# Kernel tuning notes

Measured on AMD Instinct MI355X. Metric: run time of the kernel, lower is better.

## Reference

```python
import jax, jax.numpy as jnp
import numpy as np

PIECES = 64  # self.plane


def _proj(f, w1, b1, w2, b2):
    # Projection: fc2(relu(fc1(f))), final_relu=False
    h = jax.nn.relu(f @ w1 + b1)
    return h @ w2 + b2


def _cf(img, param, pieces):
    # img: [B,3,H,W], param: [B,3,P]
    # total[b,c,h,w] = sum_i clamp(img - i/P, 0, 1/P) * param[b,c,i], then * P / sum_i param
    grid = jnp.arange(pieces, dtype=img.dtype) / pieces            # [P]
    clipped = jnp.clip(img[..., None] - grid, 0.0, 1.0 / pieces)   # [B,3,H,W,P]
    total = jnp.einsum('bchwp,bcp->bchw', clipped, param)
    norm = pieces / (jnp.sum(param, axis=-1) + 1e-30)              # [B,3]
    return total * norm[:, :, None, None]


def setup_inputs() -> dict:
    key = jax.random.key(0)
    ks = jax.random.split(key, 11)
    B, H, W = 8, 256, 256
    s = 0.05
    return {
        'x': jax.random.uniform(ks[0], (B, 3, H, W), jnp.float32),
        'f_feature': jax.random.normal(ks[1], (B, 512), jnp.float32),
        'b_feature': jax.random.normal(ks[2], (B, 512), jnp.float32),
        # stacked weights for [fc_f_1, fc_b_1, fc_f_s, fc_b_s]
        'proj_w1': jax.random.normal(ks[3], (4, 512, 192), jnp.float32) * s,
        'proj_b1': jax.random.normal(ks[4], (4, 192), jnp.float32) * s,
        'proj_w2': jax.random.normal(ks[5], (4, 192, 192), jnp.float32) * s,
        'proj_b2': jax.random.normal(ks[6], (4, 192), jnp.float32) * s,
        'fc_w1': jax.random.normal(ks[7], (576, 192), jnp.float32) * s,
        'fc_b1': jax.random.normal(ks[8], (192,), jnp.float32) * s,
        'fc_w2': jax.random.normal(ks[9], (192, 192), jnp.float32) * s,
        'fc_b2': jax.random.normal(ks[10], (192,), jnp.float32) * s,
    }


def reference(x, f_feature, b_feature, proj_w1, proj_b1, proj_w2, proj_b2,
              fc_w1, fc_b1, fc_w2, fc_b2):
    B = x.shape[0]
    # rgb_to_grayscale with 3 output channels (ITU-R 601 weights)
    gw = jnp.array([0.299, 0.587, 0.114], dtype=x.dtype)
    gray = jnp.broadcast_to(jnp.einsum('bchw,c->bhw', x, gw)[:, None], x.shape)

    # four stacked Projections: inputs [f, b, f, b]
    feats = jnp.stack([f_feature, b_feature, f_feature, b_feature])       # [4,B,512]
    h = jax.nn.relu(jnp.einsum('kbi,kio->kbo', feats, proj_w1) + proj_b1[:, None, :])
    outs = jnp.einsum('kbo,koq->kbq', h, proj_w2) + proj_b2[:, None, :]   # [4,B,192]
    param_f, param_b = outs[0], outs[1]
    param_s = outs[2] + outs[3]

    cat = jnp.concatenate([param_f, param_b, param_s], axis=1)            # [B,576]
    param = _proj(cat, fc_w1, fc_b1, fc_w2, fc_b2)                        # [B,192]

    p_all = param.reshape(B, 3, PIECES)
    p_f = param_f.reshape(B, 3, PIECES)
    p_b = param_b.reshape(B, 3, PIECES)

    return (_cf(x, p_all, PIECES), _cf(gray, p_f, PIECES), _cf(gray, p_b, PIECES))
```

## Files before the change

### kernel.cpp

```cpp
#include <hip/hip_runtime.h>

#define HWSZ 65536
#define PLANE (3 * HWSZ)
#define OUTSTRIDE (8 * PLANE)
#define MAGIC 0x13572468

__global__ __launch_bounds__(384) void k_mlp(
    const float* __restrict__ f, const float* __restrict__ bf,
    const float* __restrict__ pw1, const float* __restrict__ pb1,
    const float* __restrict__ pw2, const float* __restrict__ pb2,
    const float* __restrict__ fw1, const float* __restrict__ fb1,
    const float* __restrict__ fw2, const float* __restrict__ fb2,
    float* __restrict__ ws) {
  __shared__ float smem[2304];
  int t = threadIdx.x, blk = blockIdx.x;

  float* outs  = ws;
  float* hc    = ws + 12288;
  float* param = ws + 13824;
  int* fbase = (int*)(ws + 16384);

  int k = blk >> 3, b = blk & 7;
  {
    int q = t % 48, s = t / 48;
    float* sf  = smem;
    float* red = smem + 512;
    float* sh  = smem + 2048;

    const float* feat = ((k & 1) ? bf : f) + b * 512;
    for (int i = t; i < 512; i += 384) sf[i] = feat[i];
    __syncthreads();

    {
      const float4* w = (const float4*)(pw1 + (size_t)k * (512 * 192));
      float4 acc = {0.f, 0.f, 0.f, 0.f};
      int i0 = s * 64;
      for (int r = 0; r < 4; ++r) {
        float4 wv[16];
#pragma unroll
        for (int j = 0; j < 16; ++j)
          wv[j] = w[(size_t)(i0 + r * 16 + j) * 48 + q];
#pragma unroll
        for (int j = 0; j < 16; ++j) {
          float v = sf[i0 + r * 16 + j];
          acc.x = fmaf(v, wv[j].x, acc.x); acc.y = fmaf(v, wv[j].y, acc.y);
          acc.z = fmaf(v, wv[j].z, acc.z); acc.w = fmaf(v, wv[j].w, acc.w);
        }
      }
      ((float4*)(red + s * 192))[q] = acc;
    }
    __syncthreads();
    if (t < 192) {
      float a = pb1[k * 192 + t];
#pragma unroll
      for (int s2 = 0; s2 < 8; ++s2) a += red[s2 * 192 + t];
      sh[t] = fmaxf(a, 0.f);
    }
    __syncthreads();
    {
      const float4* w = (const float4*)(pw2 + (size_t)k * (192 * 192));
      float4 acc = {0.f, 0.f, 0.f, 0.f};
      int i0 = s * 24;
      for (int r = 0; r < 2; ++r) {
        float4 wv[12];
#pragma unroll
        for (int j = 0; j < 12; ++j)
          wv[j] = w[(size_t)(i0 + r * 12 + j) * 48 + q];
#pragma unroll
        for (int j = 0; j < 12; ++j) {
          float v = sh[i0 + r * 12 + j];
          acc.x = fmaf(v, wv[j].x, acc.x); acc.y = fmaf(v, wv[j].y, acc.y);
          acc.z = fmaf(v, wv[j].z, acc.z); acc.w = fmaf(v, wv[j].w, acc.w);
        }
      }
      ((float4*)(red + s * 192))[q] = acc;
    }
    __syncthreads();
    if (t < 192) {
      float a = pb2[k * 192 + t];
#pragma unroll
      for (int s2 = 0; s2 < 8; ++s2) a += red[s2 * 192 + t];
      outs[(k * 8 + b) * 192 + t] = a;
    }
    __syncthreads();
    if (t == 0) {
      __threadfence();
      atomicExch(&fbase[blk * 16], MAGIC);
    }
  }

  int b2 = blk & 7, c4 = blk >> 3, ob2 = c4 * 48;
  int q = t % 12, s = t / 12;

  float4 wv1[18];
  {
    const float4* w = (const float4*)fw1;
    int i0 = s * 18;
#pragma unroll
    for (int j = 0; j < 18; ++j)
      wv1[j] = w[(size_t)(i0 + j) * 48 + (ob2 >> 2) + q];
  }

  if (t < 4) {
    while (atomicAdd(&fbase[(t * 8 + b2) * 16], 0) != MAGIC)
      __builtin_amdgcn_s_sleep(2);
  }
  __syncthreads();
  if (t == 0) __threadfence();
  __syncthreads();

  {
    float* sc  = smem;
    float* red = smem + 576;
    for (int idx = t; idx < 576; idx += 384) {
      float v;
      if (idx < 192)      v = outs[(0 * 8 + b2) * 192 + idx];
      else if (idx < 384) v = outs[(1 * 8 + b2) * 192 + (idx - 192)];
      else                v = outs[(2 * 8 + b2) * 192 + (idx - 384)] +
                              outs[(3 * 8 + b2) * 192 + (idx - 384)];
      sc[idx] = v;
    }
    __syncthreads();
    float4 acc = {0.f, 0.f, 0.f, 0.f};
    int i0 = s * 18;
#pragma unroll
    for (int j = 0; j < 18; ++j) {
      float v = sc[i0 + j];
      acc.x = fmaf(v, wv1[j].x, acc.x); acc.y = fmaf(v, wv1[j].y, acc.y);
      acc.z = fmaf(v, wv1[j].z, acc.z); acc.w = fmaf(v, wv1[j].w, acc.w);
    }
    ((float4*)(red + s * 48))[q] = acc;
    __syncthreads();
    if (t < 48) {
      float a = fb1[ob2 + t];
#pragma unroll
      for (int s2 = 0; s2 < 32; ++s2) a += red[s2 * 48 + t];
      hc[b2 * 192 + ob2 + t] = fmaxf(a, 0.f);
    }
    __syncthreads();
    if (t == 0) {
      __threadfence();
      atomicExch(&fbase[(64 + blk) * 16], MAGIC);
    }
  }

  float4 wv2[6];
  {
    const float4* w = (const float4*)fw2;
    int i0 = s * 6;
#pragma unroll
    for (int j = 0; j < 6; ++j)
      wv2[j] = w[(size_t)(i0 + j) * 48 + (ob2 >> 2) + q];
  }

  if (t < 4) {
    while (atomicAdd(&fbase[(64 + t * 8 + b2) * 16], 0) != MAGIC)
      __builtin_amdgcn_s_sleep(2);
  }
  __syncthreads();
  if (t == 0) __threadfence();
  __syncthreads();

  {
    float* sh  = smem;
    float* red = smem + 576;
    if (t < 192) sh[t] = hc[b2 * 192 + t];
    __syncthreads();
    float4 acc = {0.f, 0.f, 0.f, 0.f};
    int i0 = s * 6;
#pragma unroll
    for (int j = 0; j < 6; ++j) {
      float v = sh[i0 + j];
      acc.x = fmaf(v, wv2[j].x, acc.x); acc.y = fmaf(v, wv2[j].y, acc.y);
      acc.z = fmaf(v, wv2[j].z, acc.z); acc.w = fmaf(v, wv2[j].w, acc.w);
    }
    ((float4*)(red + s * 48))[q] = acc;
    __syncthreads();
    if (t < 48) {
      float a = fb2[ob2 + t];
#pragma unroll
      for (int s2 = 0; s2 < 32; ++s2) a += red[s2 * 48 + t];
      param[b2 * 192 + ob2 + t] = a;
    }
  }
}

__global__ __launch_bounds__(256) void k_render(
    const float* __restrict__ x, const float* __restrict__ ws,
    float* __restrict__ out) {
  int b = blockIdx.y, t = threadIdx.x;
  int wave = t >> 6, lane = t & 63;
  const float* outs  = ws;
  const float* param = ws + 13824;
  __shared__ float2 tab[576];

  int s4a = blockIdx.x * 512 + t, s4b = s4a + 256;
  const float* xb = x + (size_t)b * PLANE;
  float4 vr0 = ((const float4*)(xb))[s4a];
  float4 vr1 = ((const float4*)(xb))[s4b];
  float4 vg0 = ((const float4*)(xb + HWSZ))[s4a];
  float4 vg1 = ((const float4*)(xb + HWSZ))[s4b];
  float4 vb0 = ((const float4*)(xb + 2 * HWSZ))[s4a];
  float4 vb1 = ((const float4*)(xb + 2 * HWSZ))[s4b];

  for (int cur = wave; cur < 9; cur += 4) {
    int oi = cur / 3, c = cur - oi * 3;
    const float* src = (oi == 0) ? param + b * 192 + c * 64
                                 : outs + ((oi - 1) * 8 + b) * 192 + c * 64;
    float p = src[lane];
    float v = p;
#pragma unroll
    for (int d = 1; d < 64; d <<= 1) {
      float n = __shfl_up(v, d, 64);
      if (lane >= d) v += n;
    }
    float total = __shfl(v, 63, 64);
    float norm = 64.f / (total + 1e-30f);
    tab[cur * 64 + lane] = make_float2((v - p) * 0.015625f * norm, p * norm);
  }
  __syncthreads();

  auto idx_of = [&](float v, int& kk, float& tt) {
    int k = (int)(v * 64.f);
    k = k < 0 ? 0 : (k > 63 ? 63 : k);
    kk = k;
    tt = v - (float)k * 0.015625f;
  };
  auto evk = [&](int cur, int k, float tt) -> float {
    float2 e = tab[cur * 64 + k];
    return fmaf(tt, e.y, e.x);
  };
  auto ev4 = [&](int cur, float4 v) -> float4 {
    int k; float tt; float4 r;
    idx_of(v.x, k, tt); r.x = evk(cur, k, tt);
    idx_of(v.y, k, tt); r.y = evk(cur, k, tt);
    idx_of(v.z, k, tt); r.z = evk(cur, k, tt);
    idx_of(v.w, k, tt); r.w = evk(cur, k, tt);
    return r;
  };

  float* o0 = out + (size_t)b * PLANE;
  float* o1 = out + OUTSTRIDE + (size_t)b * PLANE;
  float* o2 = out + 2 * OUTSTRIDE + (size_t)b * PLANE;

  auto process = [&](int s4, float4 vr, float4 vg, float4 vb) {
    float4 gr;
    gr.x = fmaf(0.299f, vr.x, fmaf(0.587f, vg.x, 0.114f * vb.x));
    gr.y = fmaf(0.299f, vr.y, fmaf(0.587f, vg.y, 0.114f * vb.y));
    gr.z = fmaf(0.299f, vr.z, fmaf(0.587f, vg.z, 0.114f * vb.z));
    gr.w = fmaf(0.299f, vr.w, fmaf(0.587f, vg.w, 0.114f * vb.w));

    ((float4*)(o0))[s4]            = ev4(0, vr);
    ((float4*)(o0 + HWSZ))[s4]     = ev4(1, vg);
    ((float4*)(o0 + 2 * HWSZ))[s4] = ev4(2, vb);

    int kx, ky, kz, kw; float tx, ty, tz, tw;
    idx_of(gr.x, kx, tx); idx_of(gr.y, ky, ty);
    idx_of(gr.z, kz, tz); idx_of(gr.w, kw, tw);
#pragma unroll
    for (int c = 0; c < 3; ++c) {
      float4 r;
      r.x = evk(3 + c, kx, tx); r.y = evk(3 + c, ky, ty);
      r.z = evk(3 + c, kz, tz); r.w = evk(3 + c, kw, tw);
      ((float4*)(o1 + c * HWSZ))[s4] = r;
    }
#pragma unroll
    for (int c = 0; c < 3; ++c) {
      float4 r;
      r.x = evk(6 + c, kx, tx); r.y = evk(6 + c, ky, ty);
      r.z = evk(6 + c, kz, tz); r.w = evk(6 + c, kw, tw);
      ((float4*)(o2 + c * HWSZ))[s4] = r;
    }
  };

  process(s4a, vr0, vg0, vb0);
  process(s4b, vr1, vg1, vb1);
}

extern "C" void kernel_launch(void* const* d_in, const int* in_sizes, int n_in,
                              void* d_out, int out_size, void* d_ws, size_t ws_size,
                              hipStream_t stream) {
  const float* x   = (const float*)d_in[0];
  const float* f   = (const float*)d_in[1];
  const float* bf  = (const float*)d_in[2];
  const float* pw1 = (const float*)d_in[3];
  const float* pb1 = (const float*)d_in[4];
  const float* pw2 = (const float*)d_in[5];
  const float* pb2 = (const float*)d_in[6];
  const float* fw1 = (const float*)d_in[7];
  const float* fb1 = (const float*)d_in[8];
  const float* fw2 = (const float*)d_in[9];
  const float* fb2 = (const float*)d_in[10];
  float* out = (float*)d_out;
  float* ws  = (float*)d_ws;

  k_mlp<<<32, 384, 0, stream>>>(f, bf, pw1, pb1, pw2, pb2, fw1, fb1, fw2,
                                fb2, ws);
  dim3 grid(32, 8);
  k_render<<<grid, 256, 0, stream>>>(x, ws, out);
}
```

Measured before the change: 101.5 us.

## Fuse MLP into render kernel with flag-synchronized overlap of grayscale outputs

Merges the MLP and render kernels into a single launch, assigning MLP work to one block per (bx,b) diagonal while all blocks render. Blocks first write grayscale-based outputs that depend only on the first-stage projections, then wait on per-batch flags for the final param before writing the first output. This removes a kernel launch boundary and overlaps the second MLP stages with output writing, at the cost of relying on all blocks being co-resident for spin-wait correctness and of flags persisting across calls.

```diff
diff --git a/kernel.cpp b/kernel.cpp
--- a/kernel.cpp
+++ b/kernel.cpp
@@ -5,208 +5,223 @@
 #define OUTSTRIDE (8 * PLANE)
 #define MAGIC 0x13572468
 
-__global__ __launch_bounds__(384) void k_mlp(
+__global__ __launch_bounds__(512) void k_fused(
+    const float* __restrict__ x,
     const float* __restrict__ f, const float* __restrict__ bf,
     const float* __restrict__ pw1, const float* __restrict__ pb1,
     const float* __restrict__ pw2, const float* __restrict__ pb2,
     const float* __restrict__ fw1, const float* __restrict__ fb1,
     const float* __restrict__ fw2, const float* __restrict__ fb2,
-    float* __restrict__ ws) {
+    float* __restrict__ ws, float* __restrict__ out) {
   __shared__ float smem[2304];
-  int t = threadIdx.x, blk = blockIdx.x;
+  __shared__ float2 tab[576];
+  const int t = threadIdx.x;
+  const int bx = blockIdx.x, b = blockIdx.y;
 
   float* outs  = ws;
   float* hc    = ws + 12288;
   float* param = ws + 13824;
   int* fbase = (int*)(ws + 16384);
 
-  int k = blk >> 3, b = blk & 7;
-  {
-    int q = t % 48, s = t / 48;
-    float* sf  = smem;
-    float* red = smem + 512;
-    float* sh  = smem + 2048;
-
-    const float* feat = ((k & 1) ? bf : f) + b * 512;
-    for (int i = t; i < 512; i += 384) sf[i] = feat[i];
+  const int s4 = bx * 512 + t;
+  const float* xb = x + (size_t)b * PLANE;
+  float4 vr = ((const float4*)(xb))[s4];
+  float4 vg = ((const float4*)(xb + HWSZ))[s4];
+  float4 vb = ((const float4*)(xb + 2 * HWSZ))[s4];
+
+  const bool is_mlp = ((bx & 7) == b);
+
+  if (is_mlp) {
+    const int km = bx >> 3;
+    const int blk = km * 8 + b;
+
+    {
+      int q = t % 48, s = t / 48;
+      float* sf  = smem;
+      float* red = smem + 512;
+      float* sh  = smem + 2048;
+
+      const float* feat = ((km & 1) ? bf : f) + b * 512;
+      if (t < 512) sf[t] = feat[t];
+      __syncthreads();
+      if (t < 384) {
+        const float4* w = (const float4*)(pw1 + (size_t)km * (512 * 192));
+        float4 acc = {0.f, 0.f, 0.f, 0.f};
+        int i0 = s * 64;
+        for (int r = 0; r < 4; ++r) {
+          float4 wv[16];
+#pragma unroll
+          for (int j = 0; j < 16; ++j)
+            wv[j] = w[(size_t)(i0 + r * 16 + j) * 48 + q];
+#pragma unroll
+          for (int j = 0; j < 16; ++j) {
+            float v = sf[i0 + r * 16 + j];
+            acc.x = fmaf(v, wv[j].x, acc.x); acc.y = fmaf(v, wv[j].y, acc.y);
+            acc.z = fmaf(v, wv[j].z, acc.z); acc.w = fmaf(v, wv[j].w, acc.w);
+          }
+        }
+        ((float4*)(red + s * 192))[q] = acc;
+      }
+      __syncthreads();
+      if (t < 192) {
+        float a = pb1[km * 192 + t];
+#pragma unroll
+        for (int s2 = 0; s2 < 8; ++s2) a += red[s2 * 192 + t];
+        sh[t] = fmaxf(a, 0.f);
+      }
+      __syncthreads();
+      if (t < 384) {
+        const float4* w = (const float4*)(pw2 + (size_t)km * (192 * 192));
+        float4 acc = {0.f, 0.f, 0.f, 0.f};
+        int i0 = s * 24;
+        for (int r = 0; r < 2; ++r) {
+          float4 wv[12];
+#pragma unroll
+          for (int j = 0; j < 12; ++j)
+            wv[j] = w[(size_t)(i0 + r * 12 + j) * 48 + q];
+#pragma unroll
+          for (int j = 0; j < 12; ++j) {
+            float v = sh[i0 + r * 12 + j];
+            acc.x = fmaf(v, wv[j].x, acc.x); acc.y = fmaf(v, wv[j].y, acc.y);
+            acc.z = fmaf(v, wv[j].z, acc.z); acc.w = fmaf(v, wv[j].w, acc.w);
+          }
+        }
+        ((float4*)(red + s * 192))[q] = acc;
+      }
+      __syncthreads();
+      if (t < 192) {
+        float a = pb2[km * 192 + t];
+#pragma unroll
+        for (int s2 = 0; s2 < 8; ++s2) a += red[s2 * 192 + t];
+        outs[(km * 8 + b) * 192 + t] = a;
+      }
+      __syncthreads();
+      if (t == 0) {
+        __threadfence();
+        atomicExch(&fbase[blk * 16], MAGIC);
+      }
+    }
+
+    const int b2 = b, ob2 = km * 48;
+    int qb = t % 12, sb = t / 12;
+
+    float4 wv1[18];
+    if (t < 384) {
+      const float4* w = (const float4*)fw1;
+      int i0 = sb * 18;
+#pragma unroll
+      for (int j = 0; j < 18; ++j)
+        wv1[j] = w[(size_t)(i0 + j) * 48 + (ob2 >> 2) + qb];
+    }
+
+    if (t < 4) {
+      while (atomicAdd(&fbase[(t * 8 + b2) * 16], 0) != MAGIC)
+        __builtin_amdgcn_s_sleep(2);
+    }
     __syncthreads();
+    if (t == 0) __threadfence();
+    __syncthreads();
 
     {
-      const float4* w = (const float4*)(pw1 + (size_t)k * (512 * 192));
-      float4 acc = {0.f, 0.f, 0.f, 0.f};
-      int i0 = s * 64;
-      for (int r = 0; r < 4; ++r) {
-        float4 wv[16];
-#pragma unroll
-        for (int j = 0; j < 16; ++j)
-          wv[j] = w[(size_t)(i0 + r * 16 + j) * 48 + q];
-#pragma unroll
-        for (int j = 0; j < 16; ++j) {
-          float v = sf[i0 + r * 16 + j];
-          acc.x = fmaf(v, wv[j].x, acc.x); acc.y = fmaf(v, wv[j].y, acc.y);
-          acc.z = fmaf(v, wv[j].z, acc.z); acc.w = fmaf(v, wv[j].w, acc.w);
+      float* sc  = smem;
+      float* red = smem + 576;
+      for (int idx = t; idx < 576; idx += 512) {
+        float v;
+        if (idx < 192)      v = outs[(0 * 8 + b2) * 192 + idx];
+        else if (idx < 384) v = outs[(1 * 8 + b2) * 192 + (idx - 192)];
+        else                v = outs[(2 * 8 + b2) * 192 + (idx - 384)] +
+                                outs[(3 * 8 + b2) * 192 + (idx - 384)];
+        sc[idx] = v;
+      }
+      __syncthreads();
+      if (t < 384) {
+        float4 acc = {0.f, 0.f, 0.f, 0.f};
+        int i0 = sb * 18;
+#pragma unroll
+        for (int j = 0; j < 18; ++j) {
+          float v = sc[i0 + j];
+          acc.x = fmaf(v, wv1[j].x, acc.x); acc.y = fmaf(v, wv1[j].y, acc.y);
+          acc.z = fmaf(v, wv1[j].z, acc.z); acc.w = fmaf(v, wv1[j].w, acc.w);
         }
-      }
-      ((float4*)(red + s * 192))[q] = acc;
+        ((float4*)(red + sb * 48))[qb] = acc;
+      }
+      __syncthreads();
+      if (t < 48) {
+        float a = fb1[ob2 + t];
+#pragma unroll
+        for (int s2 = 0; s2 < 32; ++s2) a += red[s2 * 48 + t];
+        hc[b2 * 192 + ob2 + t] = fmaxf(a, 0.f);
+      }
+      __syncthreads();
+      if (t == 0) {
+        __threadfence();
+        atomicExch(&fbase[(64 + blk) * 16], MAGIC);
+      }
+    }
+
+    float4 wv2[6];
+    if (t < 384) {
+      const float4* w = (const float4*)fw2;
+      int i0 = sb * 6;
+#pragma unroll
+      for (int j = 0; j < 6; ++j)
+        wv2[j] = w[(size_t)(i0 + j) * 48 + (ob2 >> 2) + qb];
+    }
+
+    if (t < 4) {
+      while (atomicAdd(&fbase[(64 + t * 8 + b2) * 16], 0) != MAGIC)
+        __builtin_amdgcn_s_sleep(2);
     }
     __syncthreads();
-    if (t < 192) {
-      float a = pb1[k * 192 + t];
-#pragma unroll
-      for (int s2 = 0; s2 < 8; ++s2) a += red[s2 * 192 + t];
-      sh[t] = fmaxf(a, 0.f);
-    }
+    if (t == 0) __threadfence();
     __syncthreads();
+
     {
-      const float4* w = (const float4*)(pw2 + (size_t)k * (192 * 192));
-      float4 acc = {0.f, 0.f, 0.f, 0.f};
-      int i0 = s * 24;
-      for (int r = 0; r < 2; ++r) {
-        float4 wv[12];
-#pragma unroll
-        for (int j = 0; j < 12; ++j)
-          wv[j] = w[(size_t)(i0 + r * 12 + j) * 48 + q];
-#pragma unroll
-        for (int j = 0; j < 12; ++j) {
-          float v = sh[i0 + r * 12 + j];
-          acc.x = fmaf(v, wv[j].x, acc.x); acc.y = fmaf(v, wv[j].y, acc.y);
-          acc.z = fmaf(v, wv[j].z, acc.z); acc.w = fmaf(v, wv[j].w, acc.w);
+      float* sh  = smem;
+      float* red = smem + 576;
+      if (t < 192) sh[t] = hc[b2 * 192 + t];
+      __syncthreads();
+      if (t < 384) {
+        float4 acc = {0.f, 0.f, 0.f, 0.f};
+        int i0 = sb * 6;
+#pragma unroll
+        for (int j = 0; j < 6; ++j) {
+          float v = sh[i0 + j];
+          acc.x = fmaf(v, wv2[j].x, acc.x); acc.y = fmaf(v, wv2[j].y, acc.y);
+          acc.z = fmaf(v, wv2[j].z, acc.z); acc.w = fmaf(v, wv2[j].w, acc.w);
         }
-      }
-      ((float4*)(red + s * 192))[q] = acc;
-    }
-    __syncthreads();
-    if (t < 192) {
-      float a = pb2[k * 192 + t];
-#pragma unroll
-      for (int s2 = 0; s2 < 8; ++s2) a += red[s2 * 192 + t];
-      outs[(k * 8 + b) * 192 + t] = a;
-    }
-    __syncthreads();
-    if (t == 0) {
-      __threadfence();
-      atomicExch(&fbase[blk * 16], MAGIC);
-    }
-  }
-
-  int b2 = blk & 7, c4 = blk >> 3, ob2 = c4 * 48;
-  int q = t % 12, s = t / 12;
-
-  float4 wv1[18];
-  {
-    const float4* w = (const float4*)fw1;
-    int i0 = s * 18;
-#pragma unroll
-    for (int j = 0; j < 18; ++j)
-      wv1[j] = w[(size_t)(i0 + j) * 48 + (ob2 >> 2) + q];
-  }
-
-  if (t < 4) {
-    while (atomicAdd(&fbase[(t * 8 + b2) * 16], 0) != MAGIC)
+        ((float4*)(red + sb * 48))[qb] = acc;
+      }
+      __syncthreads();
+      if (t < 48) {
+        float a = fb2[ob2 + t];
+#pragma unroll
+        for (int s2 = 0; s2 < 32; ++s2) a += red[s2 * 48 + t];
+        param[b2 * 192 + ob2 + t] = a;
+      }
+      __syncthreads();
+      if (t == 0) {
+        __threadfence();
+        atomicExch(&fbase[(128 + blk) * 16], MAGIC);
+      }
+    }
+  } else {
+    asm volatile("" :: "v"(vr.x), "v"(vg.x), "v"(vb.x));
+  }
+
+  if (t < 2) {
+    while (atomicAdd(&fbase[(t * 8 + b) * 16], 0) != MAGIC)
       __builtin_amdgcn_s_sleep(2);
   }
   __syncthreads();
   if (t == 0) __threadfence();
   __syncthreads();
 
-  {
-    float* sc  = smem;
-    float* red = smem + 576;
-    for (int idx = t; idx < 576; idx += 384) {
-      float v;
-      if (idx < 192)      v = outs[(0 * 8 + b2) * 192 + idx];
-      else if (idx < 384) v = outs[(1 * 8 + b2) * 192 + (idx - 192)];
-      else                v = outs[(2 * 8 + b2) * 192 + (idx - 384)] +
-                              outs[(3 * 8 + b2) * 192 + (idx - 384)];
-      sc[idx] = v;
-    }
-    __syncthreads();
-    float4 acc = {0.f, 0.f, 0.f, 0.f};
-    int i0 = s * 18;
-#pragma unroll
-    for (int j = 0; j < 18; ++j) {
-      float v = sc[i0 + j];
-      acc.x = fmaf(v, wv1[j].x, acc.x); acc.y = fmaf(v, wv1[j].y, acc.y);
-      acc.z = fmaf(v, wv1[j].z, acc.z); acc.w = fmaf(v, wv1[j].w, acc.w);
-    }
-    ((float4*)(red + s * 48))[q] = acc;
-    __syncthreads();
-    if (t < 48) {
-      float a = fb1[ob2 + t];
-#pragma unroll
-      for (int s2 = 0; s2 < 32; ++s2) a += red[s2 * 48 + t];
-      hc[b2 * 192 + ob2 + t] = fmaxf(a, 0.f);
-    }
-    __syncthreads();
-    if (t == 0) {
-      __threadfence();
-      atomicExch(&fbase[(64 + blk) * 16], MAGIC);
-    }
-  }
-
-  float4 wv2[6];
-  {
-    const float4* w = (const float4*)fw2;
-    int i0 = s * 6;
-#pragma unroll
-    for (int j = 0; j < 6; ++j)
-      wv2[j] = w[(size_t)(i0 + j) * 48 + (ob2 >> 2) + q];
-  }
-
-  if (t < 4) {
-    while (atomicAdd(&fbase[(64 + t * 8 + b2) * 16], 0) != MAGIC)
-      __builtin_amdgcn_s_sleep(2);
-  }
-  __syncthreads();
-  if (t == 0) __threadfence();
-  __syncthreads();
-
-  {
-    float* sh  = smem;
-    float* red = smem + 576;
-    if (t < 192) sh[t] = hc[b2 * 192 + t];
-    __syncthreads();
-    float4 acc = {0.f, 0.f, 0.f, 0.f};
-    int i0 = s * 6;
-#pragma unroll
-    for (int j = 0; j < 6; ++j) {
-      float v = sh[i0 + j];
-      acc.x = fmaf(v, wv2[j].x, acc.x); acc.y = fmaf(v, wv2[j].y, acc.y);
-      acc.z = fmaf(v, wv2[j].z, acc.z); acc.w = fmaf(v, wv2[j].w, acc.w);
-    }
-    ((float4*)(red + s * 48))[q] = acc;
-    __syncthreads();
-    if (t < 48) {
-      float a = fb2[ob2 + t];
-#pragma unroll
-      for (int s2 = 0; s2 < 32; ++s2) a += red[s2 * 48 + t];
-      param[b2 * 192 + ob2 + t] = a;
-    }
-  }
-}
-
-__global__ __launch_bounds__(256) void k_render(
-    const float* __restrict__ x, const float* __restrict__ ws,
-    float* __restrict__ out) {
-  int b = blockIdx.y, t = threadIdx.x;
-  int wave = t >> 6, lane = t & 63;
-  const float* outs  = ws;
-  const float* param = ws + 13824;
-  __shared__ float2 tab[576];
-
-  int s4a = blockIdx.x * 512 + t, s4b = s4a + 256;
-  const float* xb = x + (size_t)b * PLANE;
-  float4 vr0 = ((const float4*)(xb))[s4a];
-  float4 vr1 = ((const float4*)(xb))[s4b];
-  float4 vg0 = ((const float4*)(xb + HWSZ))[s4a];
-  float4 vg1 = ((const float4*)(xb + HWSZ))[s4b];
-  float4 vb0 = ((const float4*)(xb + 2 * HWSZ))[s4a];
-  float4 vb1 = ((const float4*)(xb + 2 * HWSZ))[s4b];
-
-  for (int cur = wave; cur < 9; cur += 4) {
+  const int wave = t >> 6, lane = t & 63;
+  if (wave < 6) {
+    int cur = 3 + wave;
     int oi = cur / 3, c = cur - oi * 3;
-    const float* src = (oi == 0) ? param + b * 192 + c * 64
-                                 : outs + ((oi - 1) * 8 + b) * 192 + c * 64;
+    const float* src = outs + ((oi - 1) * 8 + b) * 192 + c * 64;
     float p = src[lane];
     float v = p;
 #pragma unroll
@@ -221,39 +236,27 @@
   __syncthreads();
 
   auto idx_of = [&](float v, int& kk, float& tt) {
-    int k = (int)(v * 64.f);
-    k = k < 0 ? 0 : (k > 63 ? 63 : k);
-    kk = k;
-    tt = v - (float)k * 0.015625f;
+    int k2 = (int)(v * 64.f);
+    k2 = k2 < 0 ? 0 : (k2 > 63 ? 63 : k2);
+    kk = k2;
+    tt = v - (float)k2 * 0.015625f;
   };
-  auto evk = [&](int cur, int k, float tt) -> float {
-    float2 e = tab[cur * 64 + k];
+  auto evk = [&](int cur, int k2, float tt) -> float {
+    float2 e = tab[cur * 64 + k2];
     return fmaf(tt, e.y, e.x);
-  };
-  auto ev4 = [&](int cur, float4 v) -> float4 {
-    int k; float tt; float4 r;
-    idx_of(v.x, k, tt); r.x = evk(cur, k, tt);
-    idx_of(v.y, k, tt); r.y = evk(cur, k, tt);
-    idx_of(v.z, k, tt); r.z = evk(cur, k, tt);
-    idx_of(v.w, k, tt); r.w = evk(cur, k, tt);
-    return r;
   };
 
   float* o0 = out + (size_t)b * PLANE;
   float* o1 = out + OUTSTRIDE + (size_t)b * PLANE;
   float* o2 = out + 2 * OUTSTRIDE + (size_t)b * PLANE;
 
-  auto process = [&](int s4, float4 vr, float4 vg, float4 vb) {
+  {
     float4 gr;
     gr.x = fmaf(0.299f, vr.x, fmaf(0.587f, vg.x, 0.114f * vb.x));
     gr.y = fmaf(0.299f, vr.y, fmaf(0.587f, vg.y, 0.114f * vb.y));
     gr.z = fmaf(0.299f, vr.z, fmaf(0.587f, vg.z, 0.114f * vb.z));
     gr.w = fmaf(0.299f, vr.w, fmaf(0.587f, vg.w, 0.114f * vb.w));
 
-    ((float4*)(o0))[s4]            = ev4(0, vr);
-    ((float4*)(o0 + HWSZ))[s4]     = ev4(1, vg);
-    ((float4*)(o0 + 2 * HWSZ))[s4] = ev4(2, vb);
-
     int kx, ky, kz, kw; float tx, ty, tz, tw;
     idx_of(gr.x, kx, tx); idx_of(gr.y, ky, ty);
     idx_of(gr.z, kz, tz); idx_of(gr.w, kw, tw);
@@ -271,10 +274,44 @@
       r.z = evk(6 + c, kz, tz); r.w = evk(6 + c, kw, tw);
       ((float4*)(o2 + c * HWSZ))[s4] = r;
     }
-  };
-
-  process(s4a, vr0, vg0, vb0);
-  process(s4b, vr1, vg1, vb1);
+  }
+
+  if (t < 4) {
+    while (atomicAdd(&fbase[(128 + t * 8 + b) * 16], 0) != MAGIC)
+      __builtin_amdgcn_s_sleep(2);
+  }
+  __syncthreads();
+  if (t == 0) __threadfence();
+  __syncthreads();
+
+  if (wave < 3) {
+    const float* src = param + b * 192 + wave * 64;
+    float p = src[lane];
+    float v = p;
+#pragma unroll
+    for (int d = 1; d < 64; d <<= 1) {
+      float n = __shfl_up(v, d, 64);
+      if (lane >= d) v += n;
+    }
+    float total = __shfl(v, 63, 64);
+    float norm = 64.f / (total + 1e-30f);
+    tab[wave * 64 + lane] = make_float2((v - p) * 0.015625f * norm, p * norm);
+  }
+  __syncthreads();
+
+  {
+    auto ev4 = [&](int cur, float4 v4) -> float4 {
+      int k2; float tt; float4 r;
+      idx_of(v4.x, k2, tt); r.x = evk(cur, k2, tt);
+      idx_of(v4.y, k2, tt); r.y = evk(cur, k2, tt);
+      idx_of(v4.z, k2, tt); r.z = evk(cur, k2, tt);
+      idx_of(v4.w, k2, tt); r.w = evk(cur, k2, tt);
+      return r;
+    };
+    ((float4*)(o0))[s4]            = ev4(0, vr);
+    ((float4*)(o0 + HWSZ))[s4]     = ev4(1, vg);
+    ((float4*)(o0 + 2 * HWSZ))[s4] = ev4(2, vb);
+  }
 }
 
 extern "C" void kernel_launch(void* const* d_in, const int* in_sizes, int n_in,
@@ -294,8 +331,7 @@
   float* out = (float*)d_out;
   float* ws  = (float*)d_ws;
 
-  k_mlp<<<32, 384, 0, stream>>>(f, bf, pw1, pb1, pw2, pb2, fw1, fb1, fw2,
-                                fb2, ws);
   dim3 grid(32, 8);
-  k_render<<<grid, 256, 0, stream>>>(x, ws, out);
+  k_fused<<<grid, 512, 0, stream>>>(x, f, bf, pw1, pb1, pw2, pb2,
+                                    fw1, fb1, fw2, fb2, ws, out);
 }
```

After: 110.1 us. +8.5%, slower.

## Remove second inter-block barrier by splitting fc2 over K and summing partials in render

Applied to the files above, without the earlier changes.

Each MLP block now computes the fc2 contribution of its own 48 hidden units across all 192 outputs and writes a partial sum. The render kernel adds the four partials when it builds its table. This drops the second cross-block spin-wait and the global round trip through the hidden buffer. In exchange the render kernel does four loads per parameter, and the fc2 weights are prefetched earlier, which raises register pressure.

```diff
diff --git a/kernel.cpp b/kernel.cpp
--- a/kernel.cpp
+++ b/kernel.cpp
@@ -15,9 +15,8 @@
   __shared__ float smem[2304];
   int t = threadIdx.x, blk = blockIdx.x;
 
-  float* outs  = ws;
-  float* hc    = ws + 12288;
-  float* param = ws + 13824;
+  float* outs    = ws;
+  float* partial = ws + 8192;
   int* fbase = (int*)(ws + 16384);
 
   int k = blk >> 3, b = blk & 7;
@@ -91,6 +90,7 @@
 
   int b2 = blk & 7, c4 = blk >> 3, ob2 = c4 * 48;
   int q = t % 12, s = t / 12;
+  int q2 = t % 48, s2 = t / 48;
 
   float4 wv1[18];
   {
@@ -99,6 +99,13 @@
 #pragma unroll
     for (int j = 0; j < 18; ++j)
       wv1[j] = w[(size_t)(i0 + j) * 48 + (ob2 >> 2) + q];
+  }
+  float4 wv2[6];
+  {
+    const float4* w = (const float4*)fw2;
+#pragma unroll
+    for (int j = 0; j < 6; ++j)
+      wv2[j] = w[(size_t)(ob2 + s2 * 6 + j) * 48 + q2];
   }
 
   if (t < 4) {
@@ -121,66 +128,41 @@
       sc[idx] = v;
     }
     __syncthreads();
-    float4 acc = {0.f, 0.f, 0.f, 0.f};
-    int i0 = s * 18;
-#pragma unroll
-    for (int j = 0; j < 18; ++j) {
-      float v = sc[i0 + j];
-      acc.x = fmaf(v, wv1[j].x, acc.x); acc.y = fmaf(v, wv1[j].y, acc.y);
-      acc.z = fmaf(v, wv1[j].z, acc.z); acc.w = fmaf(v, wv1[j].w, acc.w);
-    }
-    ((float4*)(red + s * 48))[q] = acc;
+    {
+      float4 acc = {0.f, 0.f, 0.f, 0.f};
+      int i0 = s * 18;
+#pragma unroll
+      for (int j = 0; j < 18; ++j) {
+        float v = sc[i0 + j];
+        acc.x = fmaf(v, wv1[j].x, acc.x); acc.y = fmaf(v, wv1[j].y, acc.y);
+        acc.z = fmaf(v, wv1[j].z, acc.z); acc.w = fmaf(v, wv1[j].w, acc.w);
+      }
+      ((float4*)(red + s * 48))[q] = acc;
+    }
     __syncthreads();
     if (t < 48) {
       float a = fb1[ob2 + t];
 #pragma unroll
-      for (int s2 = 0; s2 < 32; ++s2) a += red[s2 * 48 + t];
-      hc[b2 * 192 + ob2 + t] = fmaxf(a, 0.f);
-    }
-    __syncthreads();
-    if (t == 0) {
-      __threadfence();
-      atomicExch(&fbase[(64 + blk) * 16], MAGIC);
-    }
-  }
-
-  float4 wv2[6];
-  {
-    const float4* w = (const float4*)fw2;
-    int i0 = s * 6;
-#pragma unroll
-    for (int j = 0; j < 6; ++j)
-      wv2[j] = w[(size_t)(i0 + j) * 48 + (ob2 >> 2) + q];
-  }
-
-  if (t < 4) {
-    while (atomicAdd(&fbase[(64 + t * 8 + b2) * 16], 0) != MAGIC)
-      __builtin_amdgcn_s_sleep(2);
-  }
-  __syncthreads();
-  if (t == 0) __threadfence();
-  __syncthreads();
-
-  {
-    float* sh  = smem;
-    float* red = smem + 576;
-    if (t < 192) sh[t] = hc[b2 * 192 + t];
-    __syncthreads();
-    float4 acc = {0.f, 0.f, 0.f, 0.f};
-    int i0 = s * 6;
-#pragma unroll
-    for (int j = 0; j < 6; ++j) {
-      float v = sh[i0 + j];
-      acc.x = fmaf(v, wv2[j].x, acc.x); acc.y = fmaf(v, wv2[j].y, acc.y);
-      acc.z = fmaf(v, wv2[j].z, acc.z); acc.w = fmaf(v, wv2[j].w, acc.w);
-    }
-    ((float4*)(red + s * 48))[q] = acc;
-    __syncthreads();
-    if (t < 48) {
-      float a = fb2[ob2 + t];
-#pragma unroll
-      for (int s2 = 0; s2 < 32; ++s2) a += red[s2 * 48 + t];
-      param[b2 * 192 + ob2 + t] = a;
+      for (int s3 = 0; s3 < 32; ++s3) a += red[s3 * 48 + t];
+      smem[t] = fmaxf(a, 0.f);
+    }
+    __syncthreads();
+    {
+      float4 acc = {0.f, 0.f, 0.f, 0.f};
+#pragma unroll
+      for (int j = 0; j < 6; ++j) {
+        float v = smem[s2 * 6 + j];
+        acc.x = fmaf(v, wv2[j].x, acc.x); acc.y = fmaf(v, wv2[j].y, acc.y);
+        acc.z = fmaf(v, wv2[j].z, acc.z); acc.w = fmaf(v, wv2[j].w, acc.w);
+      }
+      ((float4*)(red + s2 * 192))[q2] = acc;
+    }
+    __syncthreads();
+    if (t < 192) {
+      float a = (c4 == 0) ? fb2[t] : 0.f;
+#pragma unroll
+      for (int s3 = 0; s3 < 8; ++s3) a += red[s3 * 192 + t];
+      partial[(c4 * 8 + b2) * 192 + t] = a;
     }
   }
 }
@@ -190,8 +172,8 @@
     float* __restrict__ out) {
   int b = blockIdx.y, t = threadIdx.x;
   int wave = t >> 6, lane = t & 63;
-  const float* outs  = ws;
-  const float* param = ws + 13824;
+  const float* outs    = ws;
+  const float* partial = ws + 8192;
   __shared__ float2 tab[576];
 
   int s4a = blockIdx.x * 512 + t, s4b = s4a + 256;
@@ -205,9 +187,13 @@
 
   for (int cur = wave; cur < 9; cur += 4) {
     int oi = cur / 3, c = cur - oi * 3;
-    const float* src = (oi == 0) ? param + b * 192 + c * 64
-                                 : outs + ((oi - 1) * 8 + b) * 192 + c * 64;
-    float p = src[lane];
+    float p;
+    if (oi == 0) {
+      const float* pp = partial + b * 192 + c * 64;
+      p = pp[lane] + pp[1536 + lane] + pp[3072 + lane] + pp[4608 + lane];
+    } else {
+      p = outs[((oi - 1) * 8 + b) * 192 + c * 64 + lane];
+    }
     float v = p;
 #pragma unroll
     for (int d = 1; d < 64; d <<= 1) {
```

New measurement: 97.92 us. 1.04x faster.
